# Optimization experiments

Measured on AMD Instinct MI355X. Metric: run time of the kernel, lower is better.

## Reference

```python
import jax, jax.numpy as jnp
import numpy as np

N, DEG = 20000, 16
E = N * DEG
D_IN, D_HID, D_OUT, L = 1024, 512, 128, 3


def setup_inputs() -> dict:
    key = jax.random.key(0)
    ks = jax.random.split(key, 16)
    scale = 0.02
    X = jax.random.normal(ks[0], (N, D_IN), dtype=jnp.float32)
    senders = jax.random.randint(ks[1], (E,), 0, N)
    receivers = jnp.repeat(jnp.arange(N), DEG)  # sorted, every node has DEG neighbors
    inp = {"X": X, "senders": senders, "receivers": receivers}
    ki = 2
    for l in range(L):
        din = D_IN >> l
        dh = D_HID >> l
        inp[f"lw{l}"] = jax.random.normal(ks[ki], (2 * din, dh), jnp.float32) * scale; ki += 1
        inp[f"lb{l}"] = jnp.zeros((dh,), jnp.float32)
        inp[f"aw{l}"] = jax.random.normal(ks[ki], (din, dh), jnp.float32) * scale; ki += 1
        inp[f"aq{l}"] = jax.random.normal(ks[ki], (dh,), jnp.float32) * scale; ki += 1
    inp["ow"] = jax.random.normal(ks[ki], (D_HID >> (L - 1), D_OUT), jnp.float32) * scale
    inp["ob"] = jnp.zeros((D_OUT,), jnp.float32)
    return inp


def _attend(h, senders, receivers, aw, aq):
    # scores depend only on the neighbor (sender) embedding: q @ relu(W h_j)
    logits = jnp.einsum('nh,h->n', jax.nn.relu(h @ aw), aq)            # [N]
    el = logits[senders]                                               # [E]
    m = jax.ops.segment_max(el, receivers, num_segments=N)            # per-receiver max
    w = jnp.exp(el - m[receivers])                                     # [E]
    denom = jax.ops.segment_sum(w, receivers, num_segments=N)         # [N]
    msg = jax.ops.segment_sum(w[:, None] * h[senders], receivers, num_segments=N)  # [N,D]
    return msg / denom[:, None]


def reference(X, senders, receivers,
              lw0, lb0, aw0, aq0,
              lw1, lb1, aw1, aq1,
              lw2, lb2, aw2, aq2,
              ow, ob):
    params = [(lw0, lb0, aw0, aq0), (lw1, lb1, aw1, aq1), (lw2, lb2, aw2, aq2)]
    h = X
    for lw, lb, aw, aq in params:
        hN = _attend(h, senders, receivers, aw, aq)
        h = jax.nn.relu(jnp.concatenate([h, hN], axis=1) @ lw + lb)
    return h[14] @ ow + ob
```

## Files before the change

### kernel.cpp

```cpp
#include <hip/hip_runtime.h>
#include <math.h>

typedef unsigned short ushort_t;
typedef __attribute__((ext_vector_type(8))) short short8;
typedef __attribute__((ext_vector_type(4))) float f32x4;

#define NN    20000
#define DEG   16
constexpr int MAXL2 = 1 + DEG;
constexpr int MAXL1 = MAXL2 + MAXL2*DEG;
constexpr int L0PAD = 73 * 64;

__device__ __forceinline__ ushort_t f2bf(float f) {
    unsigned u = __float_as_uint(f);
    return (ushort_t)((u + 0x7FFFu + ((u >> 16) & 1u)) >> 16);
}

__device__ void transpose_tile(const float* __restrict__ W, ushort_t* __restrict__ WT,
                               int b, int nshift, int K) {
    __shared__ float tile[32][33];
    int t = threadIdx.x;
    int N = 32 << nshift;
    int bx = b & ((1 << nshift) - 1), by = b >> nshift;
    int i0 = t >> 3, j0 = (t & 7) * 4;
    int k = by * 32 + i0, n0 = bx * 32;
    float4 v = *(const float4*)(W + (size_t)k * N + n0 + j0);
    tile[i0][j0] = v.x; tile[i0][j0 + 1] = v.y; tile[i0][j0 + 2] = v.z; tile[i0][j0 + 3] = v.w;
    __syncthreads();
    int n = n0 + i0, kc = j0;
    ushort_t* p = WT + (size_t)n * K + by * 32 + kc;
    ushort4 o;
    o.x = f2bf(tile[kc][i0]);     o.y = f2bf(tile[kc + 1][i0]);
    o.z = f2bf(tile[kc + 2][i0]); o.w = f2bf(tile[kc + 3][i0]);
    *(ushort4*)p = o;
}

__global__ __launch_bounds__(256)
void k_frontier(const int* __restrict__ senders,
                int* __restrict__ list2, int* __restrict__ inv2,
                int* __restrict__ list1, int* __restrict__ inv1,
                int* __restrict__ cnts,
                const float* __restrict__ aw0, ushort_t* __restrict__ awT,
                const float* __restrict__ aw1,
                const float* __restrict__ lw1, const float* __restrict__ aw2,
                const float* __restrict__ lw2, const float* __restrict__ ow,
                float* __restrict__ dummy,
                float4* __restrict__ zp, int n4, int nzb) {
    int t = threadIdx.x;
    int bb = (int)blockIdx.x;
    if (bb > 0) {
        int b = bb - 1;
        if (b < nzb) {
            int i = b * 256 + t;
            if (i < n4) zp[i] = make_float4(0.f, 0.f, 0.f, 0.f);
            return;
        }
        b -= nzb;
        if (b < 512) { transpose_tile(aw0, awT, b, 4, 1024); return; }
        b -= 512;
        const float4* src; int base;
        if (b < 64)        { src = (const float4*)lw1; base = b * 1024; }
        else if (b < 96)   { src = (const float4*)aw1; base = (b - 64) * 1024; }
        else if (b < 104)  { src = (const float4*)aw2; base = (b - 96) * 1024; }
        else if (b < 120)  { src = (const float4*)lw2; base = (b - 104) * 1024; }
        else               { src = (const float4*)ow;  base = (b - 120) * 1024; }
        float s = 0.f;
#pragma unroll
        for (int i = 0; i < 4; i++) {
            float4 v = src[base + i * 256 + t];
            s += v.x + v.y + v.z + v.w;
        }
        if (s == 1234.5678f) dummy[0] = s;
        return;
    }
    __shared__ unsigned bm[625];
    __shared__ int cnt;
    __shared__ int lloc[MAXL2];
    auto clear = [&]() { for (int i = t; i < 625; i += 256) bm[i] = 0u; if (t == 0) cnt = 0; };
    clear(); __syncthreads();
    if (t < 17) {
        int node = (t < 16) ? senders[14 * DEG + t] : 14;
        unsigned bit = 1u << (node & 31);
        unsigned old = atomicOr(&bm[node >> 5], bit);
        if (!(old & bit)) { int p = atomicAdd(&cnt, 1); list2[p] = node; inv2[node] = p; lloc[p] = node; }
    }
    __syncthreads();
    int c2 = cnt;
    if (t == 0) cnts[2] = c2;
    __syncthreads(); clear(); __syncthreads();
    for (int i = t; i < c2 * 17; i += 256) {
        int r = i / 17, k = i - r * 17;
        int node = (k < 16) ? senders[lloc[r] * DEG + k] : lloc[r];
        unsigned bit = 1u << (node & 31);
        unsigned old = atomicOr(&bm[node >> 5], bit);
        if (!(old & bit)) { int p = atomicAdd(&cnt, 1); list1[p] = node; inv1[node] = p; }
    }
    __syncthreads();
    if (t == 0) { int c1 = cnt; cnts[1] = c1; cnts[0] = c1 * 16; }
}

__global__ __launch_bounds__(256)
void k_prep(const float* __restrict__ X, const int* __restrict__ senders,
            const int* __restrict__ list1, const int* __restrict__ cnts,
            int* __restrict__ inv0, ushort_t* __restrict__ Xg) {
    int r = blockIdx.x;
    int t = threadIdx.x;
    int rc = cnts[0];
    ushort4 o = make_ushort4(0, 0, 0, 0);
    if (r < rc) {
        int n = list1[r >> 4];
        int s = senders[n * DEG + (r & 15)];
        if (t == 0) inv0[s] = r;
        float4 v = *(const float4*)(X + (size_t)s * 1024 + t * 4);
        o.x = f2bf(v.x); o.y = f2bf(v.y); o.z = f2bf(v.z); o.w = f2bf(v.w);
    }
    *(ushort4*)(Xg + (size_t)r * 1024 + t * 4) = o;
}

__global__ __launch_bounds__(256)
void k_logits_mfma(const ushort_t* __restrict__ Xg,
                   const ushort_t* __restrict__ WT,
                   const float* __restrict__ aq, float* __restrict__ lgc,
                   const int* __restrict__ cnt, int K) {
    __shared__ short As[64 * 40];
    __shared__ short Bs0[64 * 40];
    __shared__ short Bs1[64 * 40];
    int rcnt = *cnt;
    int row0 = blockIdx.x * 64;
    if (row0 >= rcnt) return;
    int col0 = blockIdx.y * 128;
    int t = threadIdx.x;
    int w = t >> 6, lane = t & 63;

    int sr = t >> 2, sk = (t & 3) * 8;
    const ushort_t* ap  = Xg + (size_t)(row0 + sr) * K + sk;
    const ushort_t* bp0 = WT + (size_t)(col0 + sr) * K + sk;
    const ushort_t* bp1 = WT + (size_t)(col0 + 64 + sr) * K + sk;

    int fm = lane & 15, fq = lane >> 4;
    const short* arow  = As  + (w * 16 + fm) * 40 + fq * 8;
    const short* brow0 = Bs0 + fm * 40 + fq * 8;
    const short* brow1 = Bs1 + fm * 40 + fq * 8;

    f32x4 acc[2][4];
#pragma unroll
    for (int h = 0; h < 2; h++)
#pragma unroll
        for (int c = 0; c < 4; c++) acc[h][c] = (f32x4){0.f, 0.f, 0.f, 0.f};

    short8 pa  = *(const short8*)(ap);
    short8 pb0 = *(const short8*)(bp0);
    short8 pb1 = *(const short8*)(bp1);
    for (int k0 = 0; k0 < K; k0 += 32) {
        *(short8*)(As  + sr * 40 + sk) = pa;
        *(short8*)(Bs0 + sr * 40 + sk) = pb0;
        *(short8*)(Bs1 + sr * 40 + sk) = pb1;
        __syncthreads();
        if (k0 + 32 < K) {
            pa  = *(const short8*)(ap  + k0 + 32);
            pb0 = *(const short8*)(bp0 + k0 + 32);
            pb1 = *(const short8*)(bp1 + k0 + 32);
        }
        short8 af = *(const short8*)arow;
#pragma unroll
        for (int c = 0; c < 4; c++) {
            short8 b0 = *(const short8*)(brow0 + c * 16 * 40);
            acc[0][c] = __builtin_amdgcn_mfma_f32_16x16x32_bf16(af, b0, acc[0][c], 0, 0, 0);
        }
#pragma unroll
        for (int c = 0; c < 4; c++) {
            short8 b1 = *(const short8*)(brow1 + c * 16 * 40);
            acc[1][c] = __builtin_amdgcn_mfma_f32_16x16x32_bf16(af, b1, acc[1][c], 0, 0, 0);
        }
        __syncthreads();
    }

    float aqv[2][4];
#pragma unroll
    for (int h = 0; h < 2; h++)
#pragma unroll
        for (int c = 0; c < 4; c++) aqv[h][c] = aq[col0 + h * 64 + c * 16 + fm];
#pragma unroll
    for (int r = 0; r < 4; r++) {
        float v = 0.f;
#pragma unroll
        for (int h = 0; h < 2; h++)
#pragma unroll
            for (int c = 0; c < 4; c++) v += fmaxf(acc[h][c][r], 0.f) * aqv[h][c];
#pragma unroll
        for (int off = 1; off < 16; off <<= 1) v += __shfl_xor(v, off);
        if (fm == 0) atomicAdd(&lgc[row0 + w * 16 + fq * 4 + r], v);
    }
}

__global__ __launch_bounds__(256)
void k_matmul(const float* __restrict__ A1, const float* __restrict__ A2,
              const int* __restrict__ list, const int* __restrict__ inv,
              const float* __restrict__ B, const float* __restrict__ aq,
              float* __restrict__ C, const int* __restrict__ cnt,
              int amode, int omode, int K1, int K2, int NC, int KS) {
    __shared__ float As[32][68];
    __shared__ float Bs[32][64];
    __shared__ float rowsum[64];

    int rcnt = *cnt;
    int row0 = blockIdx.x * 64;
    if (row0 >= rcnt) return;
    int col0 = blockIdx.y * 64;
    int K = K1 + K2;
    int kbeg = blockIdx.z * KS;
    int kend = kbeg + KS; if (kend > K) kend = K;

    int t = threadIdx.x;
    int ty = t >> 4, tx = t & 15;
    int lr = t >> 2, kaoff = (t & 3) * 4;
    int grow = row0 + lr;
    bool rowValid = grow < rcnt;
    const float* rp1 = A1;
    const float* rp2 = A2;
    if (rowValid) {
        int hrow;
        if (amode == 0) hrow = grow;
        else { int node = list[grow]; hrow = (amode == 2) ? inv[node] : node; }
        rp1 = A1 + (size_t)hrow * K1;
        rp2 = A2 + (size_t)grow * K2;
    }
    const float* Bp = B + col0;
    int bidx0 = t, bidx1 = t + 256;

    auto loadA = [&](int k) -> float4 {
        if (!rowValid) return make_float4(0.f, 0.f, 0.f, 0.f);
        const float* src = (k < K1) ? (rp1 + k) : (rp2 + (k - K1));
        return *(const float4*)src;
    };
    auto loadB = [&](int idx, int k0) -> float4 {
        int row = idx >> 4, c4 = (idx & 15) * 4;
        return *(const float4*)(Bp + (size_t)(k0 + row) * NC + c4);
    };

    float4 pa0 = loadA(kbeg + kaoff);
    float4 pa1 = loadA(kbeg + kaoff + 16);
    float4 pb0 = loadB(bidx0, kbeg);
    float4 pb1 = loadB(bidx1, kbeg);

    float acc[4][4] = {};
    for (int k0 = kbeg; k0 < kend; k0 += 32) {
        As[kaoff + 0][lr] = pa0.x; As[kaoff + 1][lr] = pa0.y;
        As[kaoff + 2][lr] = pa0.z; As[kaoff + 3][lr] = pa0.w;
        As[kaoff + 16][lr] = pa1.x; As[kaoff + 17][lr] = pa1.y;
        As[kaoff + 18][lr] = pa1.z; As[kaoff + 19][lr] = pa1.w;
        *(float4*)&Bs[bidx0 >> 4][(bidx0 & 15) * 4] = pb0;
        *(float4*)&Bs[bidx1 >> 4][(bidx1 & 15) * 4] = pb1;
        __syncthreads();
        if (k0 + 32 < kend) {
            pa0 = loadA(k0 + 32 + kaoff);
            pa1 = loadA(k0 + 32 + kaoff + 16);
            pb0 = loadB(bidx0, k0 + 32);
            pb1 = loadB(bidx1, k0 + 32);
        }
#pragma unroll
        for (int kk = 0; kk < 32; kk++) {
            float4 a4 = *(const float4*)&As[kk][ty * 4];
            float4 b4 = *(const float4*)&Bs[kk][tx * 4];
            float a[4] = {a4.x, a4.y, a4.z, a4.w};
            float b[4] = {b4.x, b4.y, b4.z, b4.w};
#pragma unroll
            for (int i = 0; i < 4; i++)
#pragma unroll
                for (int j = 0; j < 4; j++) acc[i][j] += a[i] * b[j];
        }
        __syncthreads();
    }

    if (omode == 0) {
#pragma unroll
        for (int i = 0; i < 4; i++) {
            int r = row0 + ty * 4 + i;
            if (r < rcnt) {
                float* Crow = C + (size_t)r * NC + col0 + tx * 4;
#pragma unroll
                for (int j = 0; j < 4; j++) atomicAdd(&Crow[j], acc[i][j]);
            }
        }
    } else {
        if (t < 64) rowsum[t] = 0.f;
        __syncthreads();
        float aqv[4];
#pragma unroll
        for (int j = 0; j < 4; j++) aqv[j] = aq[col0 + tx * 4 + j];
#pragma unroll
        for (int i = 0; i < 4; i++) {
            float s = 0.f;
#pragma unroll
            for (int j = 0; j < 4; j++) {
                float v = acc[i][j];
                v = v > 0.f ? v : 0.f;
                s += v * aqv[j];
            }
            atomicAdd(&rowsum[ty * 4 + i], s);
        }
        __syncthreads();
        if (t < 64) {
            int r = row0 + t;
            if (r < rcnt) atomicAdd(&C[r], rowsum[t]);
        }
    }
}

__global__ __launch_bounds__(256)
void k_bias_logits(const float* __restrict__ C0, const float* __restrict__ lb0,
                   const float* __restrict__ aw1, const float* __restrict__ aq1,
                   float* __restrict__ h1, float* __restrict__ lgc1,
                   const int* __restrict__ cnt) {
    __shared__ float sh[512];
    __shared__ float red[4];
    int r = blockIdx.x;
    if (r >= *cnt) return;
    int t = threadIdx.x;
    float v0 = C0[(size_t)r * 512 + t] + lb0[t];
    float v1 = C0[(size_t)r * 512 + 256 + t] + lb0[256 + t];
    v0 = v0 > 0.f ? v0 : 0.f;
    v1 = v1 > 0.f ? v1 : 0.f;
    sh[t] = v0; sh[256 + t] = v1;
    h1[(size_t)r * 512 + t] = v0;
    h1[(size_t)r * 512 + 256 + t] = v1;
    __syncthreads();
    float dot = 0.f;
    for (int k = 0; k < 512; k += 4) {
        dot += sh[k + 0] * aw1[(size_t)(k + 0) * 256 + t]
             + sh[k + 1] * aw1[(size_t)(k + 1) * 256 + t]
             + sh[k + 2] * aw1[(size_t)(k + 2) * 256 + t]
             + sh[k + 3] * aw1[(size_t)(k + 3) * 256 + t];
    }
    float v = (dot > 0.f ? dot : 0.f) * aq1[t];
#pragma unroll
    for (int off = 1; off < 64; off <<= 1) v += __shfl_xor(v, off);
    if ((t & 63) == 0) red[t >> 6] = v;
    __syncthreads();
    if (t == 0) lgc1[r] = red[0] + red[1] + red[2] + red[3];
}

__global__ __launch_bounds__(256)
void k_agg(const float* __restrict__ Hsrc, const int* __restrict__ invH,
           const float* __restrict__ lgc, const int* __restrict__ invL,
           const int* __restrict__ senders,
           const int* __restrict__ listN, const int* __restrict__ cntN,
           float* __restrict__ hN, int din) {
    __shared__ int   s_row[DEG];
    __shared__ float s_w[DEG];
    __shared__ float s_scale;
    int b = blockIdx.x;
    if (b >= *cntN) return;
    int n = listN[b];
    int t = threadIdx.x;
    if (t < DEG) {
        int s = senders[n * DEG + t];
        s_row[t] = invH ? invH[s] : s;
        s_w[t] = lgc[invL ? invL[s] : s];
    }
    __syncthreads();
    if (t == 0) {
        float m = -1e30f;
        for (int k = 0; k < DEG; k++) m = fmaxf(m, s_w[k]);
        float d = 0.f;
        for (int k = 0; k < DEG; k++) { float w = __expf(s_w[k] - m); s_w[k] = w; d += w; }
        s_scale = 1.f / d;
    }
    __syncthreads();
    float scale = s_scale;
    for (int dI = t * 4; dI < din; dI += 1024) {
        float4 acc = make_float4(0.f, 0.f, 0.f, 0.f);
#pragma unroll
        for (int k = 0; k < DEG; k++) {
            float w = s_w[k];
            float4 v = *(const float4*)(Hsrc + (size_t)s_row[k] * din + dI);
            acc.x += w * v.x; acc.y += w * v.y; acc.z += w * v.z; acc.w += w * v.w;
        }
        acc.x *= scale; acc.y *= scale; acc.z *= scale; acc.w *= scale;
        *(float4*)(hN + (size_t)b * din + dI) = acc;
    }
}

__global__ __launch_bounds__(256)
void k_tail1(const float* __restrict__ h1, const float* __restrict__ lgc1,
             const int* __restrict__ senders, const int* __restrict__ list2,
             const int* __restrict__ inv1, const int* __restrict__ cnts,
             const float* __restrict__ lw1, const float* __restrict__ lb1,
             float* __restrict__ h2) {
    __shared__ __align__(16) float As[17][1024];
    __shared__ float sw[17][16];
    __shared__ int   srow[17][16];
    __shared__ int   orow[17];
    __shared__ float psum[8][17 * 32];
    int c2 = cnts[2];
    int t = threadIdx.x;
    int b = blockIdx.x;

    for (int i = t; i < c2 * 16; i += 256) {
        int j = i >> 4, k = i & 15;
        int s = senders[list2[j] * DEG + k];
        int rr = inv1[s];
        srow[j][k] = rr;
        sw[j][k] = lgc1[rr];
    }
    if (t < c2) orow[t] = inv1[list2[t]];
    __syncthreads();
    if (t < c2) {
        float m = -1e30f;
        for (int k = 0; k < 16; k++) m = fmaxf(m, sw[t][k]);
        float d = 0.f;
        for (int k = 0; k < 16; k++) { float w = __expf(sw[t][k] - m); sw[t][k] = w; d += w; }
        float inv = 1.f / d;
        for (int k = 0; k < 16; k++) sw[t][k] *= inv;
    }
    __syncthreads();
    for (int e = t; e < c2 * 128; e += 256) {
        int j = e >> 7, d4 = (e & 127) * 4;
        *(float4*)&As[j][d4] = *(const float4*)&h1[(size_t)orow[j] * 512 + d4];
        float4 a = make_float4(0.f, 0.f, 0.f, 0.f);
#pragma unroll
        for (int k = 0; k < 16; k++) {
            float w = sw[j][k];
            float4 v = *(const float4*)&h1[(size_t)srow[j][k] * 512 + d4];
            a.x += w * v.x; a.y += w * v.y; a.z += w * v.z; a.w += w * v.w;
        }
        *(float4*)&As[j][512 + d4] = a;
    }
    __syncthreads();
    int c = t & 31, s = t >> 5;
    int gc = b * 32 + c;
    float acc[17];
#pragma unroll
    for (int j = 0; j < 17; j++) acc[j] = 0.f;
    for (int k = s * 128; k < s * 128 + 128; k += 4) {
        float b0 = lw1[(size_t)(k + 0) * 256 + gc];
        float b1 = lw1[(size_t)(k + 1) * 256 + gc];
        float b2 = lw1[(size_t)(k + 2) * 256 + gc];
        float b3 = lw1[(size_t)(k + 3) * 256 + gc];
#pragma unroll
        for (int j = 0; j < 17; j++) {
            float4 a = *(const float4*)&As[j][k];
            acc[j] += a.x * b0 + a.y * b1 + a.z * b2 + a.w * b3;
        }
    }
#pragma unroll
    for (int j = 0; j < 17; j++) psum[s][j * 32 + c] = acc[j];
    __syncthreads();
    for (int e = t; e < c2 * 32; e += 256) {
        int j = e >> 5, cc = e & 31;
        float v = 0.f;
#pragma unroll
        for (int s2 = 0; s2 < 8; s2++) v += psum[s2][j * 32 + cc];
        v += lb1[b * 32 + cc];
        h2[(size_t)j * 256 + b * 32 + cc] = v > 0.f ? v : 0.f;
    }
}

__global__ __launch_bounds__(512)
void k_tail2(const float* __restrict__ h2, const int* __restrict__ senders,
             const int* __restrict__ inv2, const int* __restrict__ cnts,
             const float* __restrict__ aw2, const float* __restrict__ aq2,
             const float* __restrict__ lw2, const float* __restrict__ lb2,
             const float* __restrict__ ow, const float* __restrict__ ob,
             float* __restrict__ out) {
    __shared__ __align__(16) float sh2[17][256];
    __shared__ __align__(16) float psum[8][17][128];
    __shared__ __align__(16) float h3in[512];
    __shared__ __align__(16) float sh3[128];
    __shared__ __align__(16) float psumB[16][128];
    __shared__ float slog[17];
    __shared__ float swt[16];
    __shared__ int   srow2[16];
    __shared__ int   srow14;
    int c2 = cnts[2];
    int t = threadIdx.x;
    for (int e = t; e < c2 * 64; e += 512) {
        int j = e >> 6, d4 = (e & 63) * 4;
        *(float4*)&sh2[j][d4] = *(const float4*)&h2[(size_t)j * 256 + d4];
    }
    if (t < c2) slog[t] = 0.f;
    if (t < 16) srow2[t] = inv2[senders[14 * DEG + t]];
    if (t == 31) srow14 = inv2[14];
    __syncthreads();
    {
        int cg = t & 31;
        int s  = (t >> 5) & 7;
        int jg = t >> 8;
        int j0 = jg * 9;
        int jend = min(c2, j0 + 9);
        float4 acc[9];
#pragma unroll
        for (int i = 0; i < 9; i++) acc[i] = make_float4(0.f, 0.f, 0.f, 0.f);
        const float* ap = aw2 + cg * 4;
        for (int k = s * 32; k < s * 32 + 32; k++) {
            float4 bv = *(const float4*)(ap + (size_t)k * 128);
#pragma unroll
            for (int i = 0; i < 9; i++) {
                int j = j0 + i;
                if (j < jend) {
                    float a = sh2[j][k];
                    acc[i].x += a * bv.x; acc[i].y += a * bv.y;
                    acc[i].z += a * bv.z; acc[i].w += a * bv.w;
                }
            }
        }
#pragma unroll
        for (int i = 0; i < 9; i++) {
            int j = j0 + i;
            if (j < jend) *(float4*)&psum[s][j][cg * 4] = acc[i];
        }
    }
    __syncthreads();
    for (int e = t; e < c2 * 128; e += 512) {
        int j = e >> 7, c = e & 127;
        float v = 0.f;
#pragma unroll
        for (int s = 0; s < 8; s++) v += psum[s][j][c];
        v = v > 0.f ? v : 0.f;
        atomicAdd(&slog[j], v * aq2[c]);
    }
    __syncthreads();
    if (t == 0) {
        float m = -1e30f;
        for (int k = 0; k < 16; k++) m = fmaxf(m, slog[srow2[k]]);
        float d = 0.f;
        for (int k = 0; k < 16; k++) { float w = __expf(slog[srow2[k]] - m); swt[k] = w; d += w; }
        float inv = 1.f / d;
        for (int k = 0; k < 16; k++) swt[k] *= inv;
    }
    __syncthreads();
    if (t < 256) {
        float a = 0.f;
#pragma unroll
        for (int k = 0; k < 16; k++) a += swt[k] * sh2[srow2[k]][t];
        h3in[256 + t] = a;
    } else {
        int d = t - 256;
        h3in[d] = sh2[srow14][d];
    }
    __syncthreads();
    {
        int cg = t & 31, s = t >> 5;
        float4 acc = make_float4(0.f, 0.f, 0.f, 0.f);
        const float* bp = lw2 + cg * 4;
        for (int k = s * 32; k < s * 32 + 32; k++) {
            float4 bv = *(const float4*)(bp + (size_t)k * 128);
            float a = h3in[k];
            acc.x += a * bv.x; acc.y += a * bv.y; acc.z += a * bv.z; acc.w += a * bv.w;
        }
        *(float4*)&psumB[s][cg * 4] = acc;
    }
    __syncthreads();
    if (t < 128) {
        float v = lb2[t];
#pragma unroll
        for (int s = 0; s < 16; s++) v += psumB[s][t];
        sh3[t] = v > 0.f ? v : 0.f;
    }
    __syncthreads();
    {
        int cg = t & 31, s = t >> 5;
        float4 acc = make_float4(0.f, 0.f, 0.f, 0.f);
        const float* bp = ow + cg * 4;
        for (int k = s * 8; k < s * 8 + 8; k++) {
            float4 bv = *(const float4*)(bp + (size_t)k * 128);
            float a = sh3[k];
            acc.x += a * bv.x; acc.y += a * bv.y; acc.z += a * bv.z; acc.w += a * bv.w;
        }
        *(float4*)&psumB[s][cg * 4] = acc;
    }
    __syncthreads();
    if (t < 128) {
        float v = ob[t];
#pragma unroll
        for (int s = 0; s < 16; s++) v += psumB[s][t];
        out[t] = v;
    }
}

extern "C" void kernel_launch(void* const* d_in, const int* in_sizes, int n_in,
                              void* d_out, int out_size, void* d_ws, size_t ws_size,
                              hipStream_t stream) {
    const float* X       = (const float*)d_in[0];
    const int*   senders = (const int*)d_in[1];
    const float* lw0 = (const float*)d_in[3];
    const float* lb0 = (const float*)d_in[4];
    const float* aw0 = (const float*)d_in[5];
    const float* aq0 = (const float*)d_in[6];
    const float* lw1 = (const float*)d_in[7];
    const float* lb1 = (const float*)d_in[8];
    const float* aw1 = (const float*)d_in[9];
    const float* aq1 = (const float*)d_in[10];
    const float* lw2 = (const float*)d_in[11];
    const float* lb2 = (const float*)d_in[12];
    const float* aw2 = (const float*)d_in[13];
    const float* aq2 = (const float*)d_in[14];
    const float* owp = (const float*)d_in[15];
    const float* obp = (const float*)d_in[16];
    float* out = (float*)d_out;

    char* ws = (char*)d_ws;
    size_t off = 0;
    auto alloc = [&](size_t nbytes) -> void* {
        void* p = ws + off;
        off += (nbytes + 255) & ~(size_t)255;
        return p;
    };
    float* lgc0     = (float*)alloc(L0PAD * 4);
    float* C0       = (float*)alloc((size_t)MAXL1 * 512 * 4);
    size_t zero_end = off;
    float* lgc1 = (float*)alloc(MAXL1 * 4);
    int* inv0  = (int*)alloc(NN * 4);
    int* inv1  = (int*)alloc(NN * 4);
    int* inv2  = (int*)alloc(NN * 4);
    int* list1 = (int*)alloc(MAXL1 * 4);
    int* list2 = (int*)alloc(MAXL2 * 4);
    int* cnts  = (int*)alloc(4 * 4);
    float* dummy = (float*)alloc(16);
    ushort_t* Xg   = (ushort_t*)alloc((size_t)L0PAD * 1024 * 2);
    ushort_t* awT  = (ushort_t*)alloc((size_t)512 * 1024 * 2);
    float* hN0c = (float*)alloc((size_t)MAXL1 * 1024 * 4);
    float* h1c  = (float*)alloc((size_t)MAXL1 * 512 * 4);
    float* h2c  = (float*)alloc((size_t)MAXL2 * 256 * 4);
    (void)in_sizes; (void)n_in; (void)out_size; (void)ws_size;

    int nz4 = (int)(zero_end / 16);
    int nzb = (nz4 + 255) / 256;

    hipLaunchKernelGGL(k_frontier, dim3(1 + nzb + 512 + 124), dim3(256), 0, stream,
                       senders, list2, inv2, list1, inv1, cnts,
                       aw0, awT, aw1, lw1, aw2, lw2, owp, dummy,
                       (float4*)ws, nz4, nzb);
    hipLaunchKernelGGL(k_prep, dim3(L0PAD), dim3(256), 0, stream,
                       X, senders, list1, cnts, inv0, Xg);
    hipLaunchKernelGGL(k_logits_mfma, dim3(73, 4), dim3(256), 0, stream,
                       Xg, awT, aq0, lgc0, cnts + 0, 1024);
    hipLaunchKernelGGL(k_agg, dim3(MAXL1), dim3(256), 0, stream,
                       X, (const int*)nullptr, lgc0, inv0, senders, list1, cnts + 1, hN0c, 1024);
    hipLaunchKernelGGL(k_matmul, dim3((MAXL1 + 63) / 64, 512 / 64, 8), dim3(256), 0, stream,
                       X, hN0c, list1, (int*)nullptr, lw0, aq0, C0, cnts + 1,
                       1, 0, 1024, 1024, 512, 256);
    hipLaunchKernelGGL(k_bias_logits, dim3(MAXL1), dim3(256), 0, stream,
                       C0, lb0, aw1, aq1, h1c, lgc1, cnts + 1);
    hipLaunchKernelGGL(k_tail1, dim3(8), dim3(256), 0, stream,
                       h1c, lgc1, senders, list2, inv1, cnts, lw1, lb1, h2c);
    hipLaunchKernelGGL(k_tail2, dim3(1), dim3(512), 0, stream,
                       h2c, senders, inv2, cnts, aw2, aq2, lw2, lb2, owp, obp, out);
}
```

Baseline: 267.1 us.

## Fuse gather+bf16 convert into logits GEMM, split-K partials without atomics

Removes the k_prep kernel by gathering neighbor rows of X directly inside the MFMA logits kernel and converting to bf16 on the fly with packed conversion. Layer-0 aggregation uses the row index directly instead of inverse maps. The layer-0 matmul switches from atomicAdd into a zeroed buffer to 16-way split-K partial buffers summed in the bias kernel, which also shrinks the zeroing region. tail1 uses 16 blocks instead of 8. Costs: larger partial buffer reads and uncoalesced gathered loads in the GEMM.

```diff
diff --git a/kernel.cpp b/kernel.cpp
--- a/kernel.cpp
+++ b/kernel.cpp
@@ -7,32 +7,18 @@
 
 #define NN    20000
 #define DEG   16
-constexpr int MAXL2 = 1 + DEG;
-constexpr int MAXL1 = MAXL2 + MAXL2*DEG;
+constexpr int MAXL2 = 17;
+constexpr int MAXL1 = 289;
 constexpr int L0PAD = 73 * 64;
 
 __device__ __forceinline__ ushort_t f2bf(float f) {
     unsigned u = __float_as_uint(f);
     return (ushort_t)((u + 0x7FFFu + ((u >> 16) & 1u)) >> 16);
 }
-
-__device__ void transpose_tile(const float* __restrict__ W, ushort_t* __restrict__ WT,
-                               int b, int nshift, int K) {
-    __shared__ float tile[32][33];
-    int t = threadIdx.x;
-    int N = 32 << nshift;
-    int bx = b & ((1 << nshift) - 1), by = b >> nshift;
-    int i0 = t >> 3, j0 = (t & 7) * 4;
-    int k = by * 32 + i0, n0 = bx * 32;
-    float4 v = *(const float4*)(W + (size_t)k * N + n0 + j0);
-    tile[i0][j0] = v.x; tile[i0][j0 + 1] = v.y; tile[i0][j0 + 2] = v.z; tile[i0][j0 + 3] = v.w;
-    __syncthreads();
-    int n = n0 + i0, kc = j0;
-    ushort_t* p = WT + (size_t)n * K + by * 32 + kc;
-    ushort4 o;
-    o.x = f2bf(tile[kc][i0]);     o.y = f2bf(tile[kc + 1][i0]);
-    o.z = f2bf(tile[kc + 2][i0]); o.w = f2bf(tile[kc + 3][i0]);
-    *(ushort4*)p = o;
+__device__ __forceinline__ unsigned pkbf(float lo, float hi) {
+    unsigned r;
+    asm("v_cvt_pk_bf16_f32 %0, %1, %2" : "=v"(r) : "v"(lo), "v"(hi));
+    return r;
 }
 
 __global__ __launch_bounds__(256)
@@ -56,7 +42,20 @@
             return;
         }
         b -= nzb;
-        if (b < 512) { transpose_tile(aw0, awT, b, 4, 1024); return; }
+        if (b < 512) {
+            __shared__ float tile[32][33];
+            int bx = b & 15, by = b >> 4;
+            int i0 = t >> 3, j0 = (t & 7) * 4;
+            float4 v = *(const float4*)(aw0 + (size_t)(by * 32 + i0) * 512 + bx * 32 + j0);
+            tile[i0][j0] = v.x; tile[i0][j0 + 1] = v.y; tile[i0][j0 + 2] = v.z; tile[i0][j0 + 3] = v.w;
+            __syncthreads();
+            int n = bx * 32 + i0, kc = j0;
+            ushort4 o;
+            o.x = f2bf(tile[kc][i0]);     o.y = f2bf(tile[kc + 1][i0]);
+            o.z = f2bf(tile[kc + 2][i0]); o.w = f2bf(tile[kc + 3][i0]);
+            *(ushort4*)(awT + (size_t)n * 1024 + by * 32 + kc) = o;
+            return;
+        }
         b -= 512;
         const float4* src; int base;
         if (b < 64)        { src = (const float4*)lw1; base = b * 1024; }
@@ -100,28 +99,10 @@
 }
 
 __global__ __launch_bounds__(256)
-void k_prep(const float* __restrict__ X, const int* __restrict__ senders,
-            const int* __restrict__ list1, const int* __restrict__ cnts,
-            int* __restrict__ inv0, ushort_t* __restrict__ Xg) {
-    int r = blockIdx.x;
-    int t = threadIdx.x;
-    int rc = cnts[0];
-    ushort4 o = make_ushort4(0, 0, 0, 0);
-    if (r < rc) {
-        int n = list1[r >> 4];
-        int s = senders[n * DEG + (r & 15)];
-        if (t == 0) inv0[s] = r;
-        float4 v = *(const float4*)(X + (size_t)s * 1024 + t * 4);
-        o.x = f2bf(v.x); o.y = f2bf(v.y); o.z = f2bf(v.z); o.w = f2bf(v.w);
-    }
-    *(ushort4*)(Xg + (size_t)r * 1024 + t * 4) = o;
-}
-
-__global__ __launch_bounds__(256)
-void k_logits_mfma(const ushort_t* __restrict__ Xg,
-                   const ushort_t* __restrict__ WT,
-                   const float* __restrict__ aq, float* __restrict__ lgc,
-                   const int* __restrict__ cnt, int K) {
+void k_logits0(const float* __restrict__ X, const int* __restrict__ senders,
+               const int* __restrict__ list1, const ushort_t* __restrict__ WT,
+               const float* __restrict__ aq, float* __restrict__ lgc,
+               const int* __restrict__ cnt) {
     __shared__ short As[64 * 40];
     __shared__ short Bs0[64 * 40];
     __shared__ short Bs1[64 * 40];
@@ -131,11 +112,18 @@
     int col0 = blockIdx.y * 128;
     int t = threadIdx.x;
     int w = t >> 6, lane = t & 63;
-
     int sr = t >> 2, sk = (t & 3) * 8;
-    const ushort_t* ap  = Xg + (size_t)(row0 + sr) * K + sk;
-    const ushort_t* bp0 = WT + (size_t)(col0 + sr) * K + sk;
-    const ushort_t* bp1 = WT + (size_t)(col0 + 64 + sr) * K + sk;
+
+    int grow = row0 + sr;
+    bool av = grow < rcnt;
+    const float* xrow = X;
+    if (av) {
+        int n = list1[grow >> 4];
+        int s = senders[n * DEG + (grow & 15)];
+        xrow = X + (size_t)s * 1024;
+    }
+    const ushort_t* bp0 = WT + (size_t)(col0 + sr) * 1024 + sk;
+    const ushort_t* bp1 = WT + (size_t)(col0 + 64 + sr) * 1024 + sk;
 
     int fm = lane & 15, fq = lane >> 4;
     const short* arow  = As  + (w * 16 + fm) * 40 + fq * 8;
@@ -148,16 +136,21 @@
 #pragma unroll
         for (int c = 0; c < 4; c++) acc[h][c] = (f32x4){0.f, 0.f, 0.f, 0.f};
 
-    short8 pa  = *(const short8*)(ap);
-    short8 pb0 = *(const short8*)(bp0);
-    short8 pb1 = *(const short8*)(bp1);
-    for (int k0 = 0; k0 < K; k0 += 32) {
-        *(short8*)(As  + sr * 40 + sk) = pa;
+    float4 z4 = make_float4(0.f, 0.f, 0.f, 0.f);
+    float4 pa0 = av ? *(const float4*)(xrow + sk)     : z4;
+    float4 pa1 = av ? *(const float4*)(xrow + sk + 4) : z4;
+    short8 pb0 = *(const short8*)bp0;
+    short8 pb1 = *(const short8*)bp1;
+    for (int k0 = 0; k0 < 1024; k0 += 32) {
+        uint4 ua = make_uint4(pkbf(pa0.x, pa0.y), pkbf(pa0.z, pa0.w),
+                              pkbf(pa1.x, pa1.y), pkbf(pa1.z, pa1.w));
+        *(uint4*)(As + sr * 40 + sk) = ua;
         *(short8*)(Bs0 + sr * 40 + sk) = pb0;
         *(short8*)(Bs1 + sr * 40 + sk) = pb1;
         __syncthreads();
-        if (k0 + 32 < K) {
-            pa  = *(const short8*)(ap  + k0 + 32);
+        if (k0 + 32 < 1024) {
+            pa0 = av ? *(const float4*)(xrow + k0 + 32 + sk)     : z4;
+            pa1 = av ? *(const float4*)(xrow + k0 + 32 + sk + 4) : z4;
             pb0 = *(const short8*)(bp0 + k0 + 32);
             pb1 = *(const short8*)(bp1 + k0 + 32);
         }
@@ -194,57 +187,79 @@
 }
 
 __global__ __launch_bounds__(256)
-void k_matmul(const float* __restrict__ A1, const float* __restrict__ A2,
-              const int* __restrict__ list, const int* __restrict__ inv,
-              const float* __restrict__ B, const float* __restrict__ aq,
-              float* __restrict__ C, const int* __restrict__ cnt,
-              int amode, int omode, int K1, int K2, int NC, int KS) {
+void k_agg0(const float* __restrict__ X, const float* __restrict__ lgc0,
+            const int* __restrict__ senders, const int* __restrict__ list1,
+            const int* __restrict__ cnt1, float* __restrict__ hN0) {
+    __shared__ int   s_row[DEG];
+    __shared__ float s_w[DEG];
+    __shared__ float s_sc;
+    int b = blockIdx.x;
+    if (b >= *cnt1) return;
+    int t = threadIdx.x;
+    if (t < DEG) {
+        s_row[t] = senders[list1[b] * DEG + t];
+        s_w[t]   = lgc0[b * DEG + t];
+    }
+    __syncthreads();
+    if (t == 0) {
+        float m = -1e30f;
+        for (int k = 0; k < DEG; k++) m = fmaxf(m, s_w[k]);
+        float d = 0.f;
+        for (int k = 0; k < DEG; k++) { float w = __expf(s_w[k] - m); s_w[k] = w; d += w; }
+        s_sc = 1.f / d;
+    }
+    __syncthreads();
+    float scale = s_sc;
+    int dI = t * 4;
+    float4 acc = make_float4(0.f, 0.f, 0.f, 0.f);
+#pragma unroll
+    for (int k = 0; k < DEG; k++) {
+        float w = s_w[k];
+        float4 v = *(const float4*)(X + (size_t)s_row[k] * 1024 + dI);
+        acc.x += w * v.x; acc.y += w * v.y; acc.z += w * v.z; acc.w += w * v.w;
+    }
+    acc.x *= scale; acc.y *= scale; acc.z *= scale; acc.w *= scale;
+    *(float4*)(hN0 + (size_t)b * 1024 + dI) = acc;
+}
+
+__global__ __launch_bounds__(256)
+void k_mm0(const float* __restrict__ X, const float* __restrict__ hN0,
+           const int* __restrict__ list1, const float* __restrict__ B,
+           float* __restrict__ C0p, const int* __restrict__ cnt) {
     __shared__ float As[32][68];
     __shared__ float Bs[32][64];
-    __shared__ float rowsum[64];
-
     int rcnt = *cnt;
     int row0 = blockIdx.x * 64;
     if (row0 >= rcnt) return;
     int col0 = blockIdx.y * 64;
-    int K = K1 + K2;
-    int kbeg = blockIdx.z * KS;
-    int kend = kbeg + KS; if (kend > K) kend = K;
-
+    int kbeg = blockIdx.z * 128;
     int t = threadIdx.x;
     int ty = t >> 4, tx = t & 15;
     int lr = t >> 2, kaoff = (t & 3) * 4;
     int grow = row0 + lr;
     bool rowValid = grow < rcnt;
-    const float* rp1 = A1;
-    const float* rp2 = A2;
-    if (rowValid) {
-        int hrow;
-        if (amode == 0) hrow = grow;
-        else { int node = list[grow]; hrow = (amode == 2) ? inv[node] : node; }
-        rp1 = A1 + (size_t)hrow * K1;
-        rp2 = A2 + (size_t)grow * K2;
-    }
-    const float* Bp = B + col0;
+    const float* rp;
+    if (kbeg < 1024) rp = rowValid ? X + (size_t)list1[grow] * 1024 + kbeg : X;
+    else             rp = rowValid ? hN0 + (size_t)grow * 1024 + (kbeg - 1024) : hN0;
+    const float* Bp = B + (size_t)kbeg * 512 + col0;
     int bidx0 = t, bidx1 = t + 256;
 
     auto loadA = [&](int k) -> float4 {
         if (!rowValid) return make_float4(0.f, 0.f, 0.f, 0.f);
-        const float* src = (k < K1) ? (rp1 + k) : (rp2 + (k - K1));
-        return *(const float4*)src;
+        return *(const float4*)(rp + k);
     };
     auto loadB = [&](int idx, int k0) -> float4 {
         int row = idx >> 4, c4 = (idx & 15) * 4;
-        return *(const float4*)(Bp + (size_t)(k0 + row) * NC + c4);
+        return *(const float4*)(Bp + (size_t)(k0 + row) * 512 + c4);
     };
 
-    float4 pa0 = loadA(kbeg + kaoff);
-    float4 pa1 = loadA(kbeg + kaoff + 16);
-    float4 pb0 = loadB(bidx0, kbeg);
-    float4 pb1 = loadB(bidx1, kbeg);
+    float4 pa0 = loadA(kaoff);
+    float4 pa1 = loadA(kaoff + 16);
+    float4 pb0 = loadB(bidx0, 0);
+    float4 pb1 = loadB(bidx1, 0);
 
     float acc[4][4] = {};
-    for (int k0 = kbeg; k0 < kend; k0 += 32) {
+    for (int k0 = 0; k0 < 128; k0 += 32) {
         As[kaoff + 0][lr] = pa0.x; As[kaoff + 1][lr] = pa0.y;
         As[kaoff + 2][lr] = pa0.z; As[kaoff + 3][lr] = pa0.w;
         As[kaoff + 16][lr] = pa1.x; As[kaoff + 17][lr] = pa1.y;
@@ -252,7 +267,7 @@
         *(float4*)&Bs[bidx0 >> 4][(bidx0 & 15) * 4] = pb0;
         *(float4*)&Bs[bidx1 >> 4][(bidx1 & 15) * 4] = pb1;
         __syncthreads();
-        if (k0 + 32 < kend) {
+        if (k0 + 32 < 128) {
             pa0 = loadA(k0 + 32 + kaoff);
             pa1 = loadA(k0 + 32 + kaoff + 16);
             pb0 = loadB(bidx0, k0 + 32);
@@ -271,44 +286,18 @@
         }
         __syncthreads();
     }
-
-    if (omode == 0) {
-#pragma unroll
-        for (int i = 0; i < 4; i++) {
-            int r = row0 + ty * 4 + i;
-            if (r < rcnt) {
-                float* Crow = C + (size_t)r * NC + col0 + tx * 4;
-#pragma unroll
-                for (int j = 0; j < 4; j++) atomicAdd(&Crow[j], acc[i][j]);
-            }
-        }
-    } else {
-        if (t < 64) rowsum[t] = 0.f;
-        __syncthreads();
-        float aqv[4];
-#pragma unroll
-        for (int j = 0; j < 4; j++) aqv[j] = aq[col0 + tx * 4 + j];
-#pragma unroll
-        for (int i = 0; i < 4; i++) {
-            float s = 0.f;
-#pragma unroll
-            for (int j = 0; j < 4; j++) {
-                float v = acc[i][j];
-                v = v > 0.f ? v : 0.f;
-                s += v * aqv[j];
-            }
-            atomicAdd(&rowsum[ty * 4 + i], s);
-        }
-        __syncthreads();
-        if (t < 64) {
-            int r = row0 + t;
-            if (r < rcnt) atomicAdd(&C[r], rowsum[t]);
+#pragma unroll
+    for (int i = 0; i < 4; i++) {
+        int r = row0 + ty * 4 + i;
+        if (r < rcnt) {
+            float* Crow = C0p + ((size_t)blockIdx.z * MAXL1 + r) * 512 + col0 + tx * 4;
+            *(float4*)Crow = make_float4(acc[i][0], acc[i][1], acc[i][2], acc[i][3]);
         }
     }
 }
 
 __global__ __launch_bounds__(256)
-void k_bias_logits(const float* __restrict__ C0, const float* __restrict__ lb0,
+void k_bias_logits(const float* __restrict__ C0p, const float* __restrict__ lb0,
                    const float* __restrict__ aw1, const float* __restrict__ aq1,
                    float* __restrict__ h1, float* __restrict__ lgc1,
                    const int* __restrict__ cnt) {
@@ -317,8 +306,13 @@
     int r = blockIdx.x;
     if (r >= *cnt) return;
     int t = threadIdx.x;
-    float v0 = C0[(size_t)r * 512 + t] + lb0[t];
-    float v1 = C0[(size_t)r * 512 + 256 + t] + lb0[256 + t];
+    float v0 = lb0[t], v1 = lb0[256 + t];
+    const float* base = C0p + (size_t)r * 512;
+#pragma unroll
+    for (int z = 0; z < 16; z++) {
+        v0 += base[(size_t)z * MAXL1 * 512 + t];
+        v1 += base[(size_t)z * MAXL1 * 512 + 256 + t];
+    }
     v0 = v0 > 0.f ? v0 : 0.f;
     v1 = v1 > 0.f ? v1 : 0.f;
     sh[t] = v0; sh[256 + t] = v1;
@@ -338,47 +332,6 @@
     if ((t & 63) == 0) red[t >> 6] = v;
     __syncthreads();
     if (t == 0) lgc1[r] = red[0] + red[1] + red[2] + red[3];
-}
-
-__global__ __launch_bounds__(256)
-void k_agg(const float* __restrict__ Hsrc, const int* __restrict__ invH,
-           const float* __restrict__ lgc, const int* __restrict__ invL,
-           const int* __restrict__ senders,
-           const int* __restrict__ listN, const int* __restrict__ cntN,
-           float* __restrict__ hN, int din) {
-    __shared__ int   s_row[DEG];
-    __shared__ float s_w[DEG];
-    __shared__ float s_scale;
-    int b = blockIdx.x;
-    if (b >= *cntN) return;
-    int n = listN[b];
-    int t = threadIdx.x;
-    if (t < DEG) {
-        int s = senders[n * DEG + t];
-        s_row[t] = invH ? invH[s] : s;
-        s_w[t] = lgc[invL ? invL[s] : s];
-    }
-    __syncthreads();
-    if (t == 0) {
-        float m = -1e30f;
-        for (int k = 0; k < DEG; k++) m = fmaxf(m, s_w[k]);
-        float d = 0.f;
-        for (int k = 0; k < DEG; k++) { float w = __expf(s_w[k] - m); s_w[k] = w; d += w; }
-        s_scale = 1.f / d;
-    }
-    __syncthreads();
-    float scale = s_scale;
-    for (int dI = t * 4; dI < din; dI += 1024) {
-        float4 acc = make_float4(0.f, 0.f, 0.f, 0.f);
-#pragma unroll
-        for (int k = 0; k < DEG; k++) {
-            float w = s_w[k];
-            float4 v = *(const float4*)(Hsrc + (size_t)s_row[k] * din + dI);
-            acc.x += w * v.x; acc.y += w * v.y; acc.z += w * v.z; acc.w += w * v.w;
-        }
-        acc.x *= scale; acc.y *= scale; acc.z *= scale; acc.w *= scale;
-        *(float4*)(hN + (size_t)b * din + dI) = acc;
-    }
 }
 
 __global__ __launch_bounds__(256)
@@ -391,7 +344,7 @@
     __shared__ float sw[17][16];
     __shared__ int   srow[17][16];
     __shared__ int   orow[17];
-    __shared__ float psum[8][17 * 32];
+    __shared__ float psum[16][17 * 16];
     int c2 = cnts[2];
     int t = threadIdx.x;
     int b = blockIdx.x;
@@ -427,12 +380,12 @@
         *(float4*)&As[j][512 + d4] = a;
     }
     __syncthreads();
-    int c = t & 31, s = t >> 5;
-    int gc = b * 32 + c;
+    int c = t & 15, s = t >> 4;
+    int gc = b * 16 + c;
     float acc[17];
 #pragma unroll
     for (int j = 0; j < 17; j++) acc[j] = 0.f;
-    for (int k = s * 128; k < s * 128 + 128; k += 4) {
+    for (int k = s * 64; k < s * 64 + 64; k += 4) {
         float b0 = lw1[(size_t)(k + 0) * 256 + gc];
         float b1 = lw1[(size_t)(k + 1) * 256 + gc];
         float b2 = lw1[(size_t)(k + 2) * 256 + gc];
@@ -444,15 +397,15 @@
         }
     }
 #pragma unroll
-    for (int j = 0; j < 17; j++) psum[s][j * 32 + c] = acc[j];
-    __syncthreads();
-    for (int e = t; e < c2 * 32; e += 256) {
-        int j = e >> 5, cc = e & 31;
+    for (int j = 0; j < 17; j++) psum[s][j * 16 + c] = acc[j];
+    __syncthreads();
+    for (int e = t; e < c2 * 16; e += 256) {
+        int j = e >> 4, cc = e & 15;
         float v = 0.f;
 #pragma unroll
-        for (int s2 = 0; s2 < 8; s2++) v += psum[s2][j * 32 + cc];
-        v += lb1[b * 32 + cc];
-        h2[(size_t)j * 256 + b * 32 + cc] = v > 0.f ? v : 0.f;
+        for (int s2 = 0; s2 < 16; s2++) v += psum[s2][j * 16 + cc];
+        v += lb1[b * 16 + cc];
+        h2[(size_t)j * 256 + b * 16 + cc] = v > 0.f ? v : 0.f;
     }
 }
 
@@ -606,19 +559,17 @@
         off += (nbytes + 255) & ~(size_t)255;
         return p;
     };
-    float* lgc0     = (float*)alloc(L0PAD * 4);
-    float* C0       = (float*)alloc((size_t)MAXL1 * 512 * 4);
+    float* lgc0 = (float*)alloc(L0PAD * 4);
     size_t zero_end = off;
     float* lgc1 = (float*)alloc(MAXL1 * 4);
-    int* inv0  = (int*)alloc(NN * 4);
     int* inv1  = (int*)alloc(NN * 4);
     int* inv2  = (int*)alloc(NN * 4);
     int* list1 = (int*)alloc(MAXL1 * 4);
     int* list2 = (int*)alloc(MAXL2 * 4);
-    int* cnts  = (int*)alloc(4 * 4);
+    int* cnts  = (int*)alloc(16);
     float* dummy = (float*)alloc(16);
-    ushort_t* Xg   = (ushort_t*)alloc((size_t)L0PAD * 1024 * 2);
-    ushort_t* awT  = (ushort_t*)alloc((size_t)512 * 1024 * 2);
+    ushort_t* awT = (ushort_t*)alloc((size_t)512 * 1024 * 2);
+    float* C0p  = (float*)alloc((size_t)16 * MAXL1 * 512 * 4);
     float* hN0c = (float*)alloc((size_t)MAXL1 * 1024 * 4);
     float* h1c  = (float*)alloc((size_t)MAXL1 * 512 * 4);
     float* h2c  = (float*)alloc((size_t)MAXL2 * 256 * 4);
@@ -631,18 +582,15 @@
                        senders, list2, inv2, list1, inv1, cnts,
                        aw0, awT, aw1, lw1, aw2, lw2, owp, dummy,
                        (float4*)ws, nz4, nzb);
-    hipLaunchKernelGGL(k_prep, dim3(L0PAD), dim3(256), 0, stream,
-                       X, senders, list1, cnts, inv0, Xg);
-    hipLaunchKernelGGL(k_logits_mfma, dim3(73, 4), dim3(256), 0, stream,
-                       Xg, awT, aq0, lgc0, cnts + 0, 1024);
-    hipLaunchKernelGGL(k_agg, dim3(MAXL1), dim3(256), 0, stream,
-                       X, (const int*)nullptr, lgc0, inv0, senders, list1, cnts + 1, hN0c, 1024);
-    hipLaunchKernelGGL(k_matmul, dim3((MAXL1 + 63) / 64, 512 / 64, 8), dim3(256), 0, stream,
-                       X, hN0c, list1, (int*)nullptr, lw0, aq0, C0, cnts + 1,
-                       1, 0, 1024, 1024, 512, 256);
+    hipLaunchKernelGGL(k_logits0, dim3(73, 4), dim3(256), 0, stream,
+                       X, senders, list1, awT, aq0, lgc0, cnts + 0);
+    hipLaunchKernelGGL(k_agg0, dim3(MAXL1), dim3(256), 0, stream,
+                       X, lgc0, senders, list1, cnts + 1, hN0c);
+    hipLaunchKernelGGL(k_mm0, dim3(5, 8, 16), dim3(256), 0, stream,
+                       X, hN0c, list1, lw0, C0p, cnts + 1);
     hipLaunchKernelGGL(k_bias_logits, dim3(MAXL1), dim3(256), 0, stream,
-                       C0, lb0, aw1, aq1, h1c, lgc1, cnts + 1);
-    hipLaunchKernelGGL(k_tail1, dim3(8), dim3(256), 0, stream,
+                       C0p, lb0, aw1, aq1, h1c, lgc1, cnts + 1);
+    hipLaunchKernelGGL(k_tail1, dim3(16), dim3(256), 0, stream,
                        h1c, lgc1, senders, list2, inv1, cnts, lw1, lb1, h2c);
     hipLaunchKernelGGL(k_tail2, dim3(1), dim3(512), 0, stream,
                        h2c, senders, inv2, cnts, aw2, aq2, lw2, lb2, owp, obp, out);
```

Result: slower. 288.4 us (+8.0%).
